# Kernel tuning notes

Hardware: AMD Instinct MI355X
Metric: run time of the kernel (lower is better)

The kernel has to match this reference:

```python
import jax, jax.numpy as jnp
from jax import lax
import numpy as np

THRESHOLD = 0.9
KHALF = 5  # conv_kernel_size; full conv width = 2*KHALF + 1 = 11


def _cif_scan(eouts, alpha_norm, elens, ylens, Lp1):
    """Vectorized-over-batch integrate-and-fire scan over time (lax.scan)."""
    B, T, D = eouts.shape
    bidx = jnp.arange(B)
    dt = eouts.dtype

    def step(carry, xs):
        alpha_accum, state, n_tok, fired = carry
        a_t, e_t, t = xs  # a_t: [B], e_t: [B,D], t: scalar int
        alpha_accum = alpha_accum + a_t
        active = (t <= elens - 1) & (n_tok < ylens)
        fire = active & (alpha_accum >= THRESHOLD)
        ak1 = 1.0 - alpha_accum
        ak2 = a_t - ak1
        # attention-weight column for time t
        aw_col = jnp.zeros((B, Lp1), dt)
        w_old = jnp.where(fire, ak1, jnp.where(active, a_t, jnp.zeros((), dt)))
        aw_col = aw_col.at[bidx, n_tok].add(w_old)
        n_new = n_tok + fire.astype(n_tok.dtype)
        aw_col = aw_col.at[bidx, n_new].add(jnp.where(fire, ak2, jnp.zeros((), dt)))
        # fired output row (set once per token slot)
        fire_val = state + ak1[:, None] * e_t
        cur = fired[bidx, n_tok]
        fired = fired.at[bidx, n_tok].set(jnp.where(fire[:, None], fire_val, cur))
        # integrate / reset state
        state = jnp.where(fire[:, None], ak2[:, None] * e_t,
                          jnp.where(active[:, None], state + a_t[:, None] * e_t, state))
        alpha_accum = jnp.where(fire, ak2, alpha_accum)
        return (alpha_accum, state, n_new, fired), aw_col

    init = (jnp.zeros((B,), dt), jnp.zeros((B, D), dt),
            jnp.zeros((B,), jnp.int32), jnp.zeros((B, Lp1, D), dt))
    xs = (jnp.swapaxes(alpha_norm, 0, 1), jnp.swapaxes(eouts, 0, 1),
          jnp.arange(T))
    (_, _, _, fired), aw_cols = lax.scan(step, init, xs)
    aws = jnp.transpose(aw_cols, (1, 2, 0))[:, None]  # [B,1,Lp1,T]
    return fired, aws


def _forward(eouts, conv_w, conv_b, proj_w, proj_b, elens, ylens, L):
    # Conv1d over time, 'same' padding: [B,T,D] -> [B,T,C]
    conv_feat = lax.conv_general_dilated(
        eouts, conv_w, window_strides=(1,), padding=[(KHALF, KHALF)],
        dimension_numbers=('NWC', 'WIO', 'NWC')) + conv_b
    alpha = jax.nn.sigmoid(conv_feat @ proj_w + proj_b)[:, :, 0]  # [B,T]
    alpha_norm = alpha / jnp.sum(alpha, axis=1, keepdims=True) \
        * ylens[:, None].astype(alpha.dtype)
    fired, aws = _cif_scan(eouts, alpha_norm, elens, ylens, L + 1)
    return fired[:, :L], alpha, aws


def setup_inputs():
    key = jax.random.key(0)
    k1, k2, k3, k4, k5 = jax.random.split(key, 5)
    B, T, D, C = 16, 2048, 512, 512
    eouts = jax.random.normal(k1, (B, T, D), jnp.float32)
    elens = jnp.maximum(jax.random.randint(k2, (B,), 0, T), T // 2).astype(jnp.int32)
    ylens = jnp.maximum(jax.random.randint(k3, (B,), 0, 128), 32).astype(jnp.int32)
    conv_w = jax.random.normal(k4, (2 * KHALF + 1, D, C), jnp.float32) * 0.02
    conv_b = jnp.zeros((C,), jnp.float32)
    proj_w = jax.random.normal(k5, (C, 1), jnp.float32) * 0.05
    proj_b = jnp.zeros((1,), jnp.float32)
    return dict(eouts=eouts, conv_w=conv_w, conv_b=conv_b,
                proj_w=proj_w, proj_b=proj_b, elens=elens, ylens=ylens)


def reference(eouts, conv_w, conv_b, proj_w, proj_b, elens, ylens):
    L = int(jnp.max(ylens))  # max_len = ylens.max(), as in the original
    return _forward(eouts, conv_w, conv_b, proj_w, proj_b, elens, ylens, L)
```

## Files before the change

kernel.cpp:

```cpp
#include <hip/hip_runtime.h>
#include <math.h>

#define KHALF 5
#define MAXF 256

__device__ inline float readlane_f(float v, int lane) {
    return __int_as_float(__builtin_amdgcn_readlane(__float_as_int(v), lane));
}

__global__ void k_prep(const float* __restrict__ conv_w, const float* __restrict__ conv_b,
                       const float* __restrict__ proj_w, const float* __restrict__ proj_b,
                       float* __restrict__ w_eff, float* __restrict__ b_eff,
                       int KD, int C,
                       float* __restrict__ aws, long long awsN, int WB, int NFILL) {
    if ((int)blockIdx.x >= WB) {
        long long N4 = awsN >> 2;
        long long gid = (long long)(blockIdx.x - WB) * 256 + threadIdx.x;
        float4 z = make_float4(0.f, 0.f, 0.f, 0.f);
        float4* a4 = reinterpret_cast<float4*>(aws);
        long long stride = (long long)NFILL * 256;
        for (long long i = gid; i < N4; i += stride) a4[i] = z;
        int tail = (int)(awsN & 3);
        if (gid < tail) aws[4 * N4 + gid] = 0.f;
        return;
    }
    int gid = blockIdx.x * blockDim.x + threadIdx.x;
    int wave = gid >> 6;
    int lane = gid & 63;
    if (wave > KD) return;
    float s = 0.f;
    if (wave < KD) {
        const float* row = conv_w + (size_t)wave * C;
        for (int c = lane * 4; c < C; c += 256) {
            float4 v = *reinterpret_cast<const float4*>(row + c);
            float4 w = *reinterpret_cast<const float4*>(proj_w + c);
            s += v.x * w.x + v.y * w.y + v.z * w.z + v.w * w.w;
        }
    } else {
        for (int c = lane; c < C; c += 64) s += conv_b[c] * proj_w[c];
    }
#pragma unroll
    for (int off = 32; off > 0; off >>= 1) s += __shfl_down(s, off, 64);
    if (lane == 0) {
        if (wave < KD) w_eff[wave] = s;
        else           b_eff[0] = s + proj_b[0];
    }
}

__global__ __launch_bounds__(256) void k_qdot(const float* __restrict__ eouts,
                                              const float* __restrict__ w_eff,
                                              float* __restrict__ q, int BT) {
    __shared__ float tile[64 * 68];
    __shared__ float wls[11 * 68];
    __shared__ float part[64 * 89];
    const int u0 = blockIdx.x * 64;
    const int rp = threadIdx.x & 31;
    const int s8 = threadIdx.x >> 5;
    float acc0[11], acc1[11];
#pragma unroll
    for (int k = 0; k < 11; ++k) { acc0[k] = 0.f; acc1[k] = 0.f; }
    for (int c = 0; c < 8; ++c) {
        __syncthreads();
#pragma unroll
        for (int it = 0; it < 4; ++it) {
            int idx = it * 256 + threadIdx.x;
            int r = idx >> 4, j4 = idx & 15;
            float4 v = *reinterpret_cast<const float4*>(
                eouts + (size_t)(u0 + r) * 512 + c * 64 + j4 * 4);
            *reinterpret_cast<float4*>(&tile[r * 68 + j4 * 4]) = v;
        }
        if (threadIdx.x < 176) {
            int k = threadIdx.x >> 4, sl = threadIdx.x & 15;
            float4 wv = *reinterpret_cast<const float4*>(
                w_eff + k * 512 + c * 64 + sl * 4);
            *reinterpret_cast<float4*>(&wls[k * 68 + sl * 4]) = wv;
        }
        __syncthreads();
#pragma unroll
        for (int j4 = 0; j4 < 2; ++j4) {
            const int dl = s8 * 8 + j4 * 4;
            float4 a0 = *reinterpret_cast<const float4*>(&tile[rp * 68 + dl]);
            float4 a1 = *reinterpret_cast<const float4*>(&tile[(rp + 32) * 68 + dl]);
#pragma unroll
            for (int k = 0; k < 11; ++k) {
                float4 wv = *reinterpret_cast<const float4*>(&wls[k * 68 + dl]);
                acc0[k] += a0.x * wv.x + a0.y * wv.y + a0.z * wv.z + a0.w * wv.w;
                acc1[k] += a1.x * wv.x + a1.y * wv.y + a1.z * wv.z + a1.w * wv.w;
            }
        }
    }
    __syncthreads();
#pragma unroll
    for (int k = 0; k < 11; ++k) {
        part[rp * 89 + s8 * 11 + k] = acc0[k];
        part[(rp + 32) * 89 + s8 * 11 + k] = acc1[k];
    }
    __syncthreads();
    if (threadIdx.x < 64) {
        int r = threadIdx.x;
        const float* p = &part[r * 89];
        float o[12];
#pragma unroll
        for (int k = 0; k < 11; ++k) {
            float s0 = (p[0 * 11 + k] + p[1 * 11 + k]) + (p[2 * 11 + k] + p[3 * 11 + k]);
            float s1 = (p[4 * 11 + k] + p[5 * 11 + k]) + (p[6 * 11 + k] + p[7 * 11 + k]);
            o[k] = s0 + s1;
        }
        o[11] = 0.f;
        float4* dst = reinterpret_cast<float4*>(q + (size_t)(u0 + r) * 12);
        dst[0] = make_float4(o[0], o[1], o[2], o[3]);
        dst[1] = make_float4(o[4], o[5], o[6], o[7]);
        dst[2] = make_float4(o[8], o[9], o[10], o[11]);
    }
}

__global__ __launch_bounds__(256) void k_sigpart(const float* __restrict__ q,
                                                 const float* __restrict__ b_eff,
                                                 float* __restrict__ alpha,
                                                 float* __restrict__ partials,
                                                 int T, int tcb) {
    __shared__ float qs[266 * 12];
    __shared__ float psm[4];
    int bx = blockIdx.x;
    int b = bx / tcb, tc = bx % tcb;
    int t0 = tc * 256;
    const float* qb = q + (size_t)b * T * 12;
    const int base = (t0 - 5) * 12;
    const int lim = T * 12;
    for (int i = threadIdx.x; i < 266 * 12; i += 256) {
        int gi = base + i;
        qs[i] = (gi >= 0 && gi < lim) ? qb[gi] : 0.f;
    }
    __syncthreads();
    int t = t0 + threadIdx.x;
    float sacc = b_eff[0];
#pragma unroll
    for (int k = 0; k < 11; ++k) sacc += qs[(threadIdx.x + k) * 12 + k];
    float al = 1.f / (1.f + expf(-sacc));
    alpha[(size_t)b * T + t] = al;
    float s = al;
    int lane = threadIdx.x & 63;
    int w = threadIdx.x >> 6;
#pragma unroll
    for (int off = 32; off > 0; off >>= 1) s += __shfl_down(s, off, 64);
    if (lane == 0) psm[w] = s;
    __syncthreads();
    if (threadIdx.x == 0) {
        float tot = 0.f;
        for (int i = 0; i < 4; ++i) tot += psm[i];
        partials[bx] = tot;
    }
}

__global__ void k_alpha(const float* __restrict__ eouts,
                        const float* __restrict__ w_eff,
                        const float* __restrict__ b_eff,
                        float* __restrict__ alpha,
                        int B, int T, int D) {
    const int W = 2 * KHALF + 1;
    int gid = blockIdx.x * blockDim.x + threadIdx.x;
    int wave = gid >> 6;
    int lane = gid & 63;
    if (wave >= B * T) return;
    int b = wave / T;
    int t = wave - b * T;
    int WD = W * D;
    int t0 = t - KHALF;
    float s = 0.f;
    if (t0 >= 0 && t0 + W <= T) {
        const float* base = eouts + ((size_t)b * T + t0) * D;
        for (int j = lane * 4; j < WD; j += 256) {
            float4 v = *reinterpret_cast<const float4*>(base + j);
            float4 w = *reinterpret_cast<const float4*>(w_eff + j);
            s += v.x * w.x + v.y * w.y + v.z * w.z + v.w * w.w;
        }
    } else {
        const float* base = eouts + (size_t)b * T * D;
        for (int j = lane; j < WD; j += 64) {
            int tt = t0 + j / D;
            if (tt >= 0 && tt < T) {
                int d = j - (j / D) * D;
                s += base[(size_t)tt * D + d] * w_eff[j];
            }
        }
    }
#pragma unroll
    for (int off = 32; off > 0; off >>= 1) s += __shfl_down(s, off, 64);
    if (lane == 0) {
        float logit = s + b_eff[0];
        alpha[(size_t)b * T + t] = 1.f / (1.f + expf(-logit));
    }
}

__global__ void k_chain(const float* __restrict__ alpha_in,
                        int use_part,
                        const float* __restrict__ partials, int npart,
                        const int* __restrict__ elens,
                        const int* __restrict__ ylens,
                        float* __restrict__ anorm,
                        int* __restrict__ n_fired,
                        int* __restrict__ fire_t,
                        float* __restrict__ fire_a1,
                        float* __restrict__ fire_a2,
                        int T, int Lp1) {
    extern __shared__ float an[];
    float* pf = an + T;
    __shared__ float sm[16];
    __shared__ float stot;
    int b = blockIdx.x;
    const float* row = alpha_in + (size_t)b * T;
    if ((T & 1023) == 0) {
        const float4* r4 = reinterpret_cast<const float4*>(row);
        float4* a4 = reinterpret_cast<float4*>(an);
        for (int i = threadIdx.x; i < (T >> 2); i += blockDim.x) a4[i] = r4[i];
    } else {
        for (int i = threadIdx.x; i < T; i += blockDim.x) an[i] = row[i];
    }
    __syncthreads();
    if (use_part) {
        if (threadIdx.x < npart && threadIdx.x < 16)
            sm[threadIdx.x] = partials[b * npart + threadIdx.x];
        __syncthreads();
        if (threadIdx.x == 0) {
            float tot = 0.f;
            if (npart <= 16) { for (int i = 0; i < npart; ++i) tot += sm[i]; }
            else { for (int i = 0; i < npart; ++i) tot += partials[b * npart + i]; }
            stot = tot;
        }
    } else {
        float s = 0.f;
        for (int i = threadIdx.x; i < T; i += blockDim.x) s += an[i];
        int lane0 = threadIdx.x & 63;
        int w0 = threadIdx.x >> 6;
#pragma unroll
        for (int off = 32; off > 0; off >>= 1) s += __shfl_down(s, off, 64);
        if (lane0 == 0) sm[w0] = s;
        __syncthreads();
        if (threadIdx.x == 0) {
            float tot = 0.f;
            int nw = blockDim.x >> 6;
            for (int i = 0; i < nw; ++i) tot += sm[i];
            stot = tot;
        }
    }
    __syncthreads();
    float ssum = stot;
    float yl = (float)ylens[b];
    float* __restrict__ anb = anorm + (size_t)b * T;
    for (int i = threadIdx.x; i < T; i += blockDim.x) {
        float v = an[i] / ssum * yl;
        an[i] = v;
        anb[i] = v;
    }
    __syncthreads();
    {
        int wv = threadIdx.x >> 6, ln = threadIdx.x & 63;
        int nchunks = (T + 63) >> 6;
        for (int c = wv; c < nchunks; c += 4) {
            int t = c * 64 + ln;
            float P = (t < T) ? an[t] : 0.f;
#pragma unroll
            for (int off = 1; off < 64; off <<= 1) {
                float tmp = __shfl_up(P, off, 64);
                if (ln >= off) P += tmp;
            }
            if (t < T) pf[t] = P;
        }
    }
    __syncthreads();
    if (threadIdx.x >= 64) return;
    int lane = threadIdx.x;
    int elen = elens[b];
    if (elen > T) elen = T;
    const int ylen = ylens[b];
    int* __restrict__ ft = fire_t + (size_t)b * Lp1;
    float* __restrict__ fa1 = fire_a1 + (size_t)b * Lp1;
    float* __restrict__ fa2 = fire_a2 + (size_t)b * Lp1;
    float accum = 0.f;
    int n = 0;
    bool done = false;
    for (int t0 = 0; t0 < elen && !done; t0 += 64) {
        int nv = elen - t0;
        if (nv > 64) nv = 64;
        bool inb = (t0 + lane < T);
        float P = inb ? pf[t0 + lane] : 0.f;
        float av = inb ? an[t0 + lane] : 0.f;
        unsigned long long validmask = (nv == 64) ? ~0ull : ((1ull << nv) - 1ull);
        float base = accum;
        int start = 0;
        while (true) {
            bool cond = (base + P >= 0.9f);
            unsigned long long bal = __ballot(cond) & validmask;
            if (start > 0) bal &= (~0ull) << start;
            if (bal == 0) break;
            int u = __builtin_ctzll(bal);
            float Pu = readlane_f(P, u);
            float au = readlane_f(av, u);
            float accum_f = base + Pu;
            float ak1 = 1.f - accum_f;
            float ak2 = au - ak1;
            if (lane == 0) { ft[n] = t0 + u; fa1[n] = ak1; fa2[n] = ak2; }
            ++n;
            if (n >= ylen) { done = true; break; }
            base = ak2 - Pu;
            start = u + 1;
            if (start >= nv) break;
        }
        if (!done) accum = base + readlane_f(P, nv - 1);
    }
    if (lane == 0) n_fired[b] = n;
}

__global__ void k_awfired(const float* __restrict__ eouts,
                          const float* __restrict__ anorm,
                          const int* __restrict__ elens,
                          const int* __restrict__ ylens,
                          const int* __restrict__ n_fired,
                          const int* __restrict__ fire_t,
                          const float* __restrict__ fire_a1,
                          const float* __restrict__ fire_a2,
                          float* __restrict__ aws,
                          float* __restrict__ fired,
                          int T, int D, int L, int Lp1,
                          int AB, int tcpb, int nLh) {
    if ((int)blockIdx.x < AB) {
        __shared__ int fts[MAXF];
        __shared__ float a1s[MAXF];
        __shared__ float a2s[MAXF];
        int b = blockIdx.x / tcpb;
        int tc = blockIdx.x % tcpb;
        int nf = n_fired[b];
        for (int i = threadIdx.x; i < nf; i += blockDim.x) {
            fts[i] = fire_t[(size_t)b * Lp1 + i];
            a1s[i] = fire_a1[(size_t)b * Lp1 + i];
            a2s[i] = fire_a2[(size_t)b * Lp1 + i];
        }
        __syncthreads();
        int t = tc * 256 + threadIdx.x;
        if (t >= T) return;
        int elen = elens[b];
        if (elen > T) elen = T;
        int ylen = ylens[b];
        if (t >= elen) return;
        int lo = 0, hi = nf;
        while (lo < hi) {
            int mid = (lo + hi) >> 1;
            if (fts[mid] < t) lo = mid + 1; else hi = mid;
        }
        int rowi = lo;
        bool isfire = (rowi < nf && fts[rowi] == t);
        float* col = aws + (size_t)b * Lp1 * T + t;
        if (isfire) {
            col[(size_t)rowi * T] = a1s[rowi];
            col[(size_t)(rowi + 1) * T] = a2s[rowi];
        } else if (rowi < ylen) {
            col[(size_t)rowi * T] = anorm[(size_t)b * T + t];
        }
    } else {
        int idx = blockIdx.x - AB;
        int b = idx / nLh;
        int j = idx % nLh;
        int half = threadIdx.x >> 7;
        int dl = threadIdx.x & 127;
        int n = 2 * j + half;
        if (n >= L) return;
        int nf = n_fired[b];
        if ((D & 3) == 0) {
            int D4 = D >> 2;
            float4* dst = reinterpret_cast<float4*>(fired + ((size_t)b * L + n) * D);
            if (n >= nf) {
                for (int d4 = dl; d4 < D4; d4 += 128)
                    dst[d4] = make_float4(0.f, 0.f, 0.f, 0.f);
                return;
            }
            int t0 = (n == 0) ? 0 : fire_t[(size_t)b * Lp1 + n - 1];
            int t1 = fire_t[(size_t)b * Lp1 + n];
            float ak1 = fire_a1[(size_t)b * Lp1 + n];
            float ak2p = (n > 0) ? fire_a2[(size_t)b * Lp1 + n - 1] : 0.f;
            const float* an_g = anorm + (size_t)b * T;
            const float4* ebase = reinterpret_cast<const float4*>(
                eouts + ((size_t)b * T + t0) * D);
            for (int d4 = dl; d4 < D4; d4 += 128) {
                const float4* e = ebase + d4;
                float4 accv;
                if (t1 == t0) {
                    float4 v = e[0];
                    accv.x = ak1 * v.x; accv.y = ak1 * v.y;
                    accv.z = ak1 * v.z; accv.w = ak1 * v.w;
                } else {
                    float w0 = (n > 0) ? ak2p : an_g[t0];
                    float4 v = e[0];
                    accv.x = w0 * v.x; accv.y = w0 * v.y;
                    accv.z = w0 * v.z; accv.w = w0 * v.w;
                    float4 a0 = make_float4(0.f, 0.f, 0.f, 0.f);
                    float4 a1 = a0, a2 = a0, a3 = a0;
                    int t = t0 + 1;
                    const float4* ee = e + D4;
                    for (; t + 3 < t1; t += 4, ee += 4 * (size_t)D4) {
                        float wa = an_g[t], wb = an_g[t + 1];
                        float wc = an_g[t + 2], wd = an_g[t + 3];
                        float4 va = ee[0], vb = ee[D4], vc = ee[2 * (size_t)D4], vd = ee[3 * (size_t)D4];
                        a0.x += wa * va.x; a0.y += wa * va.y; a0.z += wa * va.z; a0.w += wa * va.w;
                        a1.x += wb * vb.x; a1.y += wb * vb.y; a1.z += wb * vb.z; a1.w += wb * vb.w;
                        a2.x += wc * vc.x; a2.y += wc * vc.y; a2.z += wc * vc.z; a2.w += wc * vc.w;
                        a3.x += wd * vd.x; a3.y += wd * vd.y; a3.z += wd * vd.z; a3.w += wd * vd.w;
                    }
                    for (; t < t1; ++t, ee += D4) {
                        float wa = an_g[t];
                        float4 va = ee[0];
                        a0.x += wa * va.x; a0.y += wa * va.y; a0.z += wa * va.z; a0.w += wa * va.w;
                    }
                    accv.x += ((a0.x + a1.x) + (a2.x + a3.x));
                    accv.y += ((a0.y + a1.y) + (a2.y + a3.y));
                    accv.z += ((a0.z + a1.z) + (a2.z + a3.z));
                    accv.w += ((a0.w + a1.w) + (a2.w + a3.w));
                    float4 vl = ee[0];
                    accv.x += ak1 * vl.x; accv.y += ak1 * vl.y;
                    accv.z += ak1 * vl.z; accv.w += ak1 * vl.w;
                }
                dst[d4] = accv;
            }
        } else {
            float* dst = fired + ((size_t)b * L + n) * D;
            if (n >= nf) {
                for (int d = dl; d < D; d += 128) dst[d] = 0.f;
                return;
            }
            int t0 = (n == 0) ? 0 : fire_t[(size_t)b * Lp1 + n - 1];
            int t1 = fire_t[(size_t)b * Lp1 + n];
            float ak1 = fire_a1[(size_t)b * Lp1 + n];
            float ak2p = (n > 0) ? fire_a2[(size_t)b * Lp1 + n - 1] : 0.f;
            const float* an_g = anorm + (size_t)b * T;
            for (int d = dl; d < D; d += 128) {
                const float* e = eouts + ((size_t)b * T + t0) * D + d;
                float accv;
                if (t1 == t0) {
                    accv = ak1 * e[0];
                } else {
                    float w0 = (n > 0) ? ak2p : an_g[t0];
                    accv = w0 * e[0];
                    float a0 = 0.f, a1 = 0.f, a2 = 0.f, a3 = 0.f;
                    int t = t0 + 1;
                    const float* ee = e + D;
                    for (; t + 3 < t1; t += 4, ee += 4 * (size_t)D) {
                        a0 += an_g[t]     * ee[0];
                        a1 += an_g[t + 1] * ee[D];
                        a2 += an_g[t + 2] * ee[2 * (size_t)D];
                        a3 += an_g[t + 3] * ee[3 * (size_t)D];
                    }
                    for (; t < t1; ++t, ee += D) a0 += an_g[t] * ee[0];
                    accv += ((a0 + a1) + (a2 + a3));
                    accv += ak1 * ee[0];
                }
                dst[d] = accv;
            }
        }
    }
}

extern "C" void kernel_launch(void* const* d_in, const int* in_sizes, int n_in,
                              void* d_out, int out_size, void* d_ws, size_t ws_size,
                              hipStream_t stream) {
    const float* eouts  = (const float*)d_in[0];
    const float* conv_w = (const float*)d_in[1];
    const float* conv_b = (const float*)d_in[2];
    const float* proj_w = (const float*)d_in[3];
    const float* proj_b = (const float*)d_in[4];
    const int*   elens  = (const int*)d_in[5];
    const int*   ylens  = (const int*)d_in[6];

    const int B = in_sizes[5];
    const int C = in_sizes[2];
    const int W = 2 * KHALF + 1;
    const int D = in_sizes[1] / (W * C);
    const int T = in_sizes[0] / (B * D);
    const int L = (out_size - 2 * B * T) / (B * (D + T));
    const int Lp1 = L + 1;
    const int BT = B * T;
    const int tcb = (T + 255) / 256;

    float* out   = (float*)d_out;
    float* fired = out;
    float* alpha = out + (size_t)B * L * D;
    float* aws   = alpha + (size_t)B * T;

    char*  ws        = (char*)d_ws;
    float* w_eff     = (float*)ws;
    float* b_eff     = (float*)(ws + (size_t)W * D * 4);
    int*   n_fired   = (int*)(b_eff + 16);
    int*   fire_t    = n_fired + B + 16;
    float* fire_a1   = (float*)(fire_t + (size_t)B * Lp1 + 16);
    float* fire_a2   = fire_a1 + (size_t)B * Lp1 + 16;
    float* anorm     = fire_a2 + (size_t)B * Lp1 + 16;
    float* qbuf      = anorm + (size_t)B * T + 16;
    float* partials  = qbuf + (size_t)BT * 12 + 16;
    size_t ws_need   = (size_t)((char*)(partials + (size_t)B * tcb + 16) - ws);

    const int KD = W * D;
    {
        long long wthreads = (long long)(KD + 1) * 64;
        int WB = (int)((wthreads + 255) / 256);
        int NFILL = 2048;
        long long awsN = (long long)B * Lp1 * T;
        k_prep<<<WB + NFILL, 256, 0, stream>>>(conv_w, conv_b, proj_w, proj_b,
                                               w_eff, b_eff, KD, C,
                                               aws, awsN, WB, NFILL);
    }

    const bool fast = (ws_size >= ws_need) && (D == 512) && (C == 512) &&
                      (BT % 64 == 0) && (T % 256 == 0) && (T <= 16384) &&
                      (Lp1 <= MAXF);
    if (fast) {
        k_qdot<<<BT / 64, 256, 0, stream>>>(eouts, w_eff, qbuf, BT);
        k_sigpart<<<B * tcb, 256, 0, stream>>>(qbuf, b_eff, alpha, partials, T, tcb);
    } else {
        long long threads = (long long)BT * 64;
        int blocks = (int)((threads + 255) / 256);
        k_alpha<<<blocks, 256, 0, stream>>>(eouts, w_eff, b_eff, alpha, B, T, D);
    }

    k_chain<<<B, 256, 2 * T * sizeof(float), stream>>>(
        alpha, fast ? 1 : 0, partials, tcb,
        elens, ylens, anorm,
        n_fired, fire_t, fire_a1, fire_a2, T, Lp1);

    {
        int tcpb = (T + 255) / 256;
        int AB = B * tcpb;
        int nLh = (L + 1) / 2;
        if (nLh < 1) nLh = 1;
        int FB = B * nLh;
        k_awfired<<<AB + FB, 256, 0, stream>>>(eouts, anorm,
                                               elens, ylens, n_fired,
                                               fire_t, fire_a1, fire_a2,
                                               aws, fired, T, D, L, Lp1,
                                               AB, tcpb, nLh);
    }
}
```

Baseline: 159.9 us.

## Prefetch qdot tiles, move aws zero-fill to sigpart, split fired rows across halves

The qdot kernel now loads the next eouts/w_eff chunk into registers while computing on the current shared tile, hiding global load latency. The aws zero-fill blocks move from the prep kernel into the sigpart launch so prep runs lean ahead of qdot. The fired-row computation gives each output row its own block, splitting time steps between two halves of the block and reducing them through shared memory, which doubles parallelism over the sequential time loop at the cost of extra syncs.

```diff
diff --git a/kernel.cpp b/kernel.cpp
--- a/kernel.cpp
+++ b/kernel.cpp
@@ -59,23 +59,38 @@
     float acc0[11], acc1[11];
 #pragma unroll
     for (int k = 0; k < 11; ++k) { acc0[k] = 0.f; acc1[k] = 0.f; }
-    for (int c = 0; c < 8; ++c) {
-        __syncthreads();
+
+    float4 rv[4];
+    float4 wv;
+    auto issue = [&](int c) {
 #pragma unroll
         for (int it = 0; it < 4; ++it) {
             int idx = it * 256 + threadIdx.x;
             int r = idx >> 4, j4 = idx & 15;
-            float4 v = *reinterpret_cast<const float4*>(
+            rv[it] = *reinterpret_cast<const float4*>(
                 eouts + (size_t)(u0 + r) * 512 + c * 64 + j4 * 4);
-            *reinterpret_cast<float4*>(&tile[r * 68 + j4 * 4]) = v;
         }
         if (threadIdx.x < 176) {
             int k = threadIdx.x >> 4, sl = threadIdx.x & 15;
-            float4 wv = *reinterpret_cast<const float4*>(
+            wv = *reinterpret_cast<const float4*>(
                 w_eff + k * 512 + c * 64 + sl * 4);
+        }
+    };
+    issue(0);
+    for (int c = 0; c < 8; ++c) {
+        __syncthreads();
+#pragma unroll
+        for (int it = 0; it < 4; ++it) {
+            int idx = it * 256 + threadIdx.x;
+            int r = idx >> 4, j4 = idx & 15;
+            *reinterpret_cast<float4*>(&tile[r * 68 + j4 * 4]) = rv[it];
+        }
+        if (threadIdx.x < 176) {
+            int k = threadIdx.x >> 4, sl = threadIdx.x & 15;
             *reinterpret_cast<float4*>(&wls[k * 68 + sl * 4]) = wv;
         }
         __syncthreads();
+        if (c + 1 < 8) issue(c + 1);
 #pragma unroll
         for (int j4 = 0; j4 < 2; ++j4) {
             const int dl = s8 * 8 + j4 * 4;
@@ -83,9 +98,9 @@
             float4 a1 = *reinterpret_cast<const float4*>(&tile[(rp + 32) * 68 + dl]);
 #pragma unroll
             for (int k = 0; k < 11; ++k) {
-                float4 wv = *reinterpret_cast<const float4*>(&wls[k * 68 + dl]);
-                acc0[k] += a0.x * wv.x + a0.y * wv.y + a0.z * wv.z + a0.w * wv.w;
-                acc1[k] += a1.x * wv.x + a1.y * wv.y + a1.z * wv.z + a1.w * wv.w;
+                float4 wvv = *reinterpret_cast<const float4*>(&wls[k * 68 + dl]);
+                acc0[k] += a0.x * wvv.x + a0.y * wvv.y + a0.z * wvv.z + a0.w * wvv.w;
+                acc1[k] += a1.x * wvv.x + a1.y * wvv.y + a1.z * wvv.z + a1.w * wvv.w;
             }
         }
     }
@@ -118,7 +133,20 @@
                                                  const float* __restrict__ b_eff,
                                                  float* __restrict__ alpha,
                                                  float* __restrict__ partials,
-                                                 int T, int tcb) {
+                                                 int T, int tcb,
+                                                 float* __restrict__ aws,
+                                                 long long awsN, int SB, int NFILL) {
+    if ((int)blockIdx.x >= SB) {
+        long long N4 = awsN >> 2;
+        long long gid = (long long)(blockIdx.x - SB) * 256 + threadIdx.x;
+        float4 z = make_float4(0.f, 0.f, 0.f, 0.f);
+        float4* a4 = reinterpret_cast<float4*>(aws);
+        long long stride = (long long)NFILL * 256;
+        for (long long i = gid; i < N4; i += stride) a4[i] = z;
+        int tail = (int)(awsN & 3);
+        if (gid < tail) aws[4 * N4 + gid] = 0.f;
+        return;
+    }
     __shared__ float qs[266 * 12];
     __shared__ float psm[4];
     int bx = blockIdx.x;
@@ -322,7 +350,7 @@
                           float* __restrict__ aws,
                           float* __restrict__ fired,
                           int T, int D, int L, int Lp1,
-                          int AB, int tcpb, int nLh) {
+                          int AB, int tcpb) {
     if ((int)blockIdx.x < AB) {
         __shared__ int fts[MAXF];
         __shared__ float a1s[MAXF];
@@ -357,20 +385,21 @@
             col[(size_t)rowi * T] = anorm[(size_t)b * T + t];
         }
     } else {
+        __shared__ float4 red[128];
         int idx = blockIdx.x - AB;
-        int b = idx / nLh;
-        int j = idx % nLh;
-        int half = threadIdx.x >> 7;
+        int b = idx / L;
+        int n = idx % L;
+        int h = threadIdx.x >> 7;
         int dl = threadIdx.x & 127;
-        int n = 2 * j + half;
-        if (n >= L) return;
         int nf = n_fired[b];
         if ((D & 3) == 0) {
             int D4 = D >> 2;
             float4* dst = reinterpret_cast<float4*>(fired + ((size_t)b * L + n) * D);
             if (n >= nf) {
-                for (int d4 = dl; d4 < D4; d4 += 128)
-                    dst[d4] = make_float4(0.f, 0.f, 0.f, 0.f);
+                if (h == 0) {
+                    for (int d4 = dl; d4 < D4; d4 += 128)
+                        dst[d4] = make_float4(0.f, 0.f, 0.f, 0.f);
+                }
                 return;
             }
             int t0 = (n == 0) ? 0 : fire_t[(size_t)b * Lp1 + n - 1];
@@ -378,52 +407,50 @@
             float ak1 = fire_a1[(size_t)b * Lp1 + n];
             float ak2p = (n > 0) ? fire_a2[(size_t)b * Lp1 + n - 1] : 0.f;
             const float* an_g = anorm + (size_t)b * T;
-            const float4* ebase = reinterpret_cast<const float4*>(
-                eouts + ((size_t)b * T + t0) * D);
-            for (int d4 = dl; d4 < D4; d4 += 128) {
-                const float4* e = ebase + d4;
-                float4 accv;
-                if (t1 == t0) {
-                    float4 v = e[0];
-                    accv.x = ak1 * v.x; accv.y = ak1 * v.y;
-                    accv.z = ak1 * v.z; accv.w = ak1 * v.w;
-                } else {
-                    float w0 = (n > 0) ? ak2p : an_g[t0];
-                    float4 v = e[0];
-                    accv.x = w0 * v.x; accv.y = w0 * v.y;
-                    accv.z = w0 * v.z; accv.w = w0 * v.w;
-                    float4 a0 = make_float4(0.f, 0.f, 0.f, 0.f);
-                    float4 a1 = a0, a2 = a0, a3 = a0;
-                    int t = t0 + 1;
-                    const float4* ee = e + D4;
-                    for (; t + 3 < t1; t += 4, ee += 4 * (size_t)D4) {
-                        float wa = an_g[t], wb = an_g[t + 1];
-                        float wc = an_g[t + 2], wd = an_g[t + 3];
-                        float4 va = ee[0], vb = ee[D4], vc = ee[2 * (size_t)D4], vd = ee[3 * (size_t)D4];
-                        a0.x += wa * va.x; a0.y += wa * va.y; a0.z += wa * va.z; a0.w += wa * va.w;
-                        a1.x += wb * vb.x; a1.y += wb * vb.y; a1.z += wb * vb.z; a1.w += wb * vb.w;
-                        a2.x += wc * vc.x; a2.y += wc * vc.y; a2.z += wc * vc.z; a2.w += wc * vc.w;
-                        a3.x += wd * vd.x; a3.y += wd * vd.y; a3.z += wd * vd.z; a3.w += wd * vd.w;
+            const float4* E = reinterpret_cast<const float4*>(eouts + (size_t)b * T * D);
+            for (int d0 = 0; d0 < D4; d0 += 128) {
+                int d4 = d0 + dl;
+                float4 acc = make_float4(0.f, 0.f, 0.f, 0.f);
+                if (d4 < D4) {
+                    float4 a0 = acc, a1 = acc, a2 = acc, a3 = acc;
+                    int t = t0 + h;
+                    for (; t + 6 <= t1; t += 8) {
+                        float w0 = (t == t1) ? ak1 : ((t == t0 && n > 0) ? ak2p : an_g[t]);
+                        float w1 = (t + 2 == t1) ? ak1 : an_g[t + 2];
+                        float w2 = (t + 4 == t1) ? ak1 : an_g[t + 4];
+                        float w3 = (t + 6 == t1) ? ak1 : an_g[t + 6];
+                        float4 v0 = E[(size_t)t * D4 + d4];
+                        float4 v1 = E[(size_t)(t + 2) * D4 + d4];
+                        float4 v2 = E[(size_t)(t + 4) * D4 + d4];
+                        float4 v3 = E[(size_t)(t + 6) * D4 + d4];
+                        a0.x += w0 * v0.x; a0.y += w0 * v0.y; a0.z += w0 * v0.z; a0.w += w0 * v0.w;
+                        a1.x += w1 * v1.x; a1.y += w1 * v1.y; a1.z += w1 * v1.z; a1.w += w1 * v1.w;
+                        a2.x += w2 * v2.x; a2.y += w2 * v2.y; a2.z += w2 * v2.z; a2.w += w2 * v2.w;
+                        a3.x += w3 * v3.x; a3.y += w3 * v3.y; a3.z += w3 * v3.z; a3.w += w3 * v3.w;
                     }
-                    for (; t < t1; ++t, ee += D4) {
-                        float wa = an_g[t];
-                        float4 va = ee[0];
-                        a0.x += wa * va.x; a0.y += wa * va.y; a0.z += wa * va.z; a0.w += wa * va.w;
+                    for (; t <= t1; t += 2) {
+                        float wt = (t == t1) ? ak1 : ((t == t0 && n > 0) ? ak2p : an_g[t]);
+                        float4 v = E[(size_t)t * D4 + d4];
+                        a0.x += wt * v.x; a0.y += wt * v.y; a0.z += wt * v.z; a0.w += wt * v.w;
                     }
-                    accv.x += ((a0.x + a1.x) + (a2.x + a3.x));
-                    accv.y += ((a0.y + a1.y) + (a2.y + a3.y));
-                    accv.z += ((a0.z + a1.z) + (a2.z + a3.z));
-                    accv.w += ((a0.w + a1.w) + (a2.w + a3.w));
-                    float4 vl = ee[0];
-                    accv.x += ak1 * vl.x; accv.y += ak1 * vl.y;
-                    accv.z += ak1 * vl.z; accv.w += ak1 * vl.w;
+                    acc.x = (a0.x + a1.x) + (a2.x + a3.x);
+                    acc.y = (a0.y + a1.y) + (a2.y + a3.y);
+                    acc.z = (a0.z + a1.z) + (a2.z + a3.z);
+                    acc.w = (a0.w + a1.w) + (a2.w + a3.w);
                 }
-                dst[d4] = accv;
+                if (h == 1 && d4 < D4) red[dl] = acc;
+                __syncthreads();
+                if (h == 0 && d4 < D4) {
+                    float4 o = red[dl];
+                    acc.x += o.x; acc.y += o.y; acc.z += o.z; acc.w += o.w;
+                    dst[d4] = acc;
+                }
+                __syncthreads();
             }
         } else {
             float* dst = fired + ((size_t)b * L + n) * D;
             if (n >= nf) {
-                for (int d = dl; d < D; d += 128) dst[d] = 0.f;
+                for (int d = threadIdx.x; d < D; d += 256) dst[d] = 0.f;
                 return;
             }
             int t0 = (n == 0) ? 0 : fire_t[(size_t)b * Lp1 + n - 1];
@@ -431,7 +458,7 @@
             float ak1 = fire_a1[(size_t)b * Lp1 + n];
             float ak2p = (n > 0) ? fire_a2[(size_t)b * Lp1 + n - 1] : 0.f;
             const float* an_g = anorm + (size_t)b * T;
-            for (int d = dl; d < D; d += 128) {
+            for (int d = threadIdx.x; d < D; d += 256) {
                 const float* e = eouts + ((size_t)b * T + t0) * D + d;
                 float accv;
                 if (t1 == t0) {
@@ -497,23 +524,27 @@
     size_t ws_need   = (size_t)((char*)(partials + (size_t)B * tcb + 16) - ws);
 
     const int KD = W * D;
-    {
-        long long wthreads = (long long)(KD + 1) * 64;
-        int WB = (int)((wthreads + 255) / 256);
-        int NFILL = 2048;
-        long long awsN = (long long)B * Lp1 * T;
+    const long long awsN = (long long)B * Lp1 * T;
+    long long wthreads = (long long)(KD + 1) * 64;
+    int WB = (int)((wthreads + 255) / 256);
+    const int NFILL = 2048;
+
+    const bool fast = (ws_size >= ws_need) && (D == 512) && (C == 512) &&
+                      (BT % 64 == 0) && (T % 256 == 0) && (T <= 16384) &&
+                      (Lp1 <= MAXF);
+
+    if (fast) {
+        k_prep<<<WB, 256, 0, stream>>>(conv_w, conv_b, proj_w, proj_b,
+                                       w_eff, b_eff, KD, C,
+                                       aws, awsN, WB, 0);
+        k_qdot<<<BT / 64, 256, 0, stream>>>(eouts, w_eff, qbuf, BT);
+        int SB = B * tcb;
+        k_sigpart<<<SB + NFILL, 256, 0, stream>>>(qbuf, b_eff, alpha, partials,
+                                                  T, tcb, aws, awsN, SB, NFILL);
+    } else {
         k_prep<<<WB + NFILL, 256, 0, stream>>>(conv_w, conv_b, proj_w, proj_b,
                                                w_eff, b_eff, KD, C,
                                                aws, awsN, WB, NFILL);
-    }
-
-    const bool fast = (ws_size >= ws_need) && (D == 512) && (C == 512) &&
-                      (BT % 64 == 0) && (T % 256 == 0) && (T <= 16384) &&
-                      (Lp1 <= MAXF);
-    if (fast) {
-        k_qdot<<<BT / 64, 256, 0, stream>>>(eouts, w_eff, qbuf, BT);
-        k_sigpart<<<B * tcb, 256, 0, stream>>>(qbuf, b_eff, alpha, partials, T, tcb);
-    } else {
         long long threads = (long long)BT * 64;
         int blocks = (int)((threads + 255) / 256);
         k_alpha<<<blocks, 256, 0, stream>>>(eouts, w_eff, b_eff, alpha, B, T, D);
@@ -527,13 +558,11 @@
     {
         int tcpb = (T + 255) / 256;
         int AB = B * tcpb;
-        int nLh = (L + 1) / 2;
-        if (nLh < 1) nLh = 1;
-        int FB = B * nLh;
+        int FB = B * L;
         k_awfired<<<AB + FB, 256, 0, stream>>>(eouts, anorm,
                                                elens, ylens, n_fired,
                                                fire_t, fire_a1, fire_a2,
                                                aws, fired, T, D, L, Lp1,
-                                               AB, tcpb, nLh);
-    }
-}
+                                               AB, tcpb);
+    }
+}
```

New measurement: 172.7 us. 1.08x slower.
